# Kernel tuning notes

Hardware: AMD Instinct MI355X
Metric: run time of the kernel (lower is better)

The kernel has to match this reference:

```python
import jax, jax.numpy as jnp
import numpy as np

N_NODES = 100000
N_EDGES = 1600000
IN_FEATS = 128
HID = 128
OUT_FEATS = 64


def setup_inputs() -> dict:
    key = jax.random.key(0)
    ks = jax.random.split(key, 8)
    node_ids = jnp.arange(N_NODES, dtype=jnp.int64)
    src = jax.random.randint(ks[0], (N_EDGES,), 0, N_NODES, dtype=jnp.int64)
    dst = jax.random.randint(ks[1], (N_EDGES,), 0, N_NODES, dtype=jnp.int64)
    emb = jax.random.normal(ks[2], (N_NODES, IN_FEATS), dtype=jnp.float32)
    W1 = jax.random.normal(ks[3], (IN_FEATS, HID), dtype=jnp.float32) / np.sqrt(IN_FEATS)
    b1 = jnp.zeros((HID,), dtype=jnp.float32)
    W2 = jax.random.normal(ks[4], (HID, OUT_FEATS), dtype=jnp.float32) / np.sqrt(HID)
    b2 = jnp.zeros((OUT_FEATS,), dtype=jnp.float32)
    return {"node_ids": node_ids, "src": src, "dst": dst, "emb": emb,
            "W1": W1, "b1": b1, "W2": W2, "b2": b2}


def _sym_norms(src, dst):
    # DGL GraphConv norm='both': D_out^{-1/2} on source side, D_in^{-1/2} on dest side,
    # degrees clamped to >= 1.
    ones = jnp.ones(src.shape[0], dtype=jnp.float32)
    deg_out = jax.ops.segment_sum(ones, src, num_segments=N_NODES)
    deg_in = jax.ops.segment_sum(ones, dst, num_segments=N_NODES)
    norm_src = jnp.clip(deg_out, 1.0, None) ** -0.5  # [N]
    norm_dst = jnp.clip(deg_in, 1.0, None) ** -0.5   # [N]
    return norm_src, norm_dst


def _spmm(src, dst, h):
    # rst[dst] += h[src]  (sparse adjacency aggregation)
    return jax.ops.segment_sum(h[src], dst, num_segments=N_NODES)


def reference(node_ids, src, dst, emb, W1, b1, W2, b2):
    norm_src, norm_dst = _sym_norms(src, dst)
    h = emb[node_ids]                                   # [N, IN]
    # Layer 1 (IN -> HID, relu): weight applied after aggregation (in <= out)
    h = _spmm(src, dst, h * norm_src[:, None]) * norm_dst[:, None]
    h = jax.nn.relu(h @ W1 + b1)                        # [N, HID]
    # Dropout(0.5) is identity in eval mode.
    # Layer 2 (HID -> OUT): DGL applies weight BEFORE aggregation when in > out
    h = (h @ W2) * norm_src[:, None]                    # [N, OUT]
    h = _spmm(src, dst, h) * norm_dst[:, None] + b2
    return h
```

## Files before the change

### kernel.cpp

```cpp
#include <hip/hip_runtime.h>

#define N_N 100000
#define N_E 1600000
#define SLOTS 48
#define N_PAD 100096

#define BK_SHIFT 9
#define BK_SIZE 512
#define NBKT 196
#define MAXB 10240
#define EPB2 2048
#define NBLK2 ((N_E + EPB2 - 1) / EPB2)
#define EPT 8

#define EMBB 6250
#define WB 96

typedef unsigned short ushort_t;
typedef unsigned int uint_t;
typedef _Float16 f16x8 __attribute__((ext_vector_type(8)));
typedef float f32x4 __attribute__((ext_vector_type(4)));

__device__ __forceinline__ ushort_t f2h(float f) {
    union { _Float16 h; ushort_t u; } c; c.h = (_Float16)f; return c.u;
}

__device__ __forceinline__ void acc2h(uint_t v, float wv, float& a, float& b) {
    union { uint_t u; _Float16 h[2]; } c; c.u = v;
    a = fmaf((float)c.h[0], wv, a);
    b = fmaf((float)c.h[1], wv, b);
}

__device__ __forceinline__ void addh(uint_t v, float& a, float& b) {
    union { uint_t u; _Float16 h[2]; } c; c.u = v;
    a += (float)c.h[0];
    b += (float)c.h[1];
}

__device__ __forceinline__ uint_t packh2(float a, float b) {
    union { _Float16 h[2]; uint_t u; } p;
    p.h[0] = (_Float16)a; p.h[1] = (_Float16)b;
    return p.u;
}

__global__ void __launch_bounds__(256) k_scatter_prep(
        const int* __restrict__ src, const int* __restrict__ dst,
        int* __restrict__ cur_d, int* __restrict__ cur_s,
        uint_t* __restrict__ pe_dst, uint_t* __restrict__ pe_src,
        const float* __restrict__ emb, ushort_t* __restrict__ embf,
        const float* __restrict__ W1, const float* __restrict__ W2,
        ushort_t* __restrict__ w1f, ushort_t* __restrict__ w2f) {
    int t = threadIdx.x, blk = blockIdx.x;
    if (blk >= NBLK2) {
        int pb = blk - NBLK2;
        if (pb < EMBB) {
            int i = pb * 512 + t;
            const float4* E4 = (const float4*)emb;
            ushort4* O4 = (ushort4*)embf;
            float4 v0 = E4[i], v1 = E4[i + 256];
            ushort4 o0, o1;
            o0.x = f2h(v0.x); o0.y = f2h(v0.y); o0.z = f2h(v0.z); o0.w = f2h(v0.w);
            o1.x = f2h(v1.x); o1.y = f2h(v1.y); o1.z = f2h(v1.z); o1.w = f2h(v1.w);
            O4[i] = o0; O4[i + 256] = o1;
        } else {
            int idx = (pb - EMBB) * 256 + t;
            int j = idx & 7, l = (idx >> 3) & 63;
            int k = (l >> 4) * 8 + j;
            int n = l & 15;
            if (idx < 16384) {
                int kc = (idx >> 9) & 3, nt = idx >> 11;
                w1f[idx] = f2h(W1[(kc * 32 + k) * 128 + nt * 16 + n]);
            } else {
                int i2 = idx - 16384;
                int kc = (i2 >> 9) & 3, nt = i2 >> 11;
                w2f[i2] = f2h(W2[(kc * 32 + k) * 64 + nt * 16 + n]);
            }
        }
        return;
    }
    __shared__ int hd[NBKT], hs[NBKT], od[NBKT], os_[NBKT];
    for (int i = t; i < NBKT; i += 256) { hd[i] = 0; hs[i] = 0; }
    __syncthreads();
    int e0 = blk * EPB2;
    int myS[EPT], myD[EPT];
    uint_t myR[EPT];
#pragma unroll
    for (int i = 0; i < EPT; i++) {
        int e = e0 + t + i * 256;
        if (e < N_E) {
            int s = src[e], d = dst[e];
            myS[i] = s; myD[i] = d;
            uint_t rd = (uint_t)atomicAdd(&hd[d >> BK_SHIFT], 1);
            uint_t rs = (uint_t)atomicAdd(&hs[s >> BK_SHIFT], 1);
            myR[i] = rd | (rs << 16);
        }
    }
    __syncthreads();
    for (int i = t; i < NBKT; i += 256) {
        int c = hd[i]; od[i]  = c ? atomicAdd(&cur_d[i], c) : 0;
        c = hs[i];     os_[i] = c ? atomicAdd(&cur_s[i], c) : 0;
    }
    __syncthreads();
#pragma unroll
    for (int i = 0; i < EPT; i++) {
        int e = e0 + t + i * 256;
        if (e < N_E) {
            int s = myS[i], d = myD[i];
            int rd = od[d >> BK_SHIFT] + (int)(myR[i] & 0xffffu);
            int rs = os_[s >> BK_SHIFT] + (int)(myR[i] >> 16);
            if (rd < MAXB) pe_dst[(size_t)(d >> BK_SHIFT) * MAXB + rd] =
                               (uint_t)s | ((uint_t)(d & 511) << 17);
            if (rs < MAXB) pe_src[(size_t)(s >> BK_SHIFT) * MAXB + rs] = (uint_t)s;
        }
    }
}

__global__ void __launch_bounds__(512) k_binC(
        const uint_t* __restrict__ pe_dst, const uint_t* __restrict__ pe_src,
        const int* __restrict__ cur_d, const int* __restrict__ cur_s,
        int* __restrict__ slots, int* __restrict__ cnt,
        float* __restrict__ nd, float* __restrict__ ns) {
    int t = threadIdx.x, bb = blockIdx.x;
    __shared__ int lc[BK_SIZE];
    for (int i = t; i < BK_SIZE; i += 512) lc[i] = 0;
    __syncthreads();
    if (bb < NBKT) {
        int b = bb;
        int cb = min(cur_d[b], MAXB);
        int nbase = b << BK_SHIFT;
        const uint_t* pe = pe_dst + (size_t)b * MAXB;
        for (int e = t; e < cb; e += 512) {
            uint_t ed = pe[e];
            int dloc = (int)(ed >> 17);
            int s = (int)(ed & 0x1ffffu);
            int pos = atomicAdd(&lc[dloc], 1);
            if (pos < SLOTS) slots[(size_t)(nbase + dloc) * SLOTS + pos] = s;
        }
        __syncthreads();
        for (int i = t; i < BK_SIZE; i += 512) {
            int n = nbase + i;
            if (n < N_N) {
                int c = lc[i];
                cnt[n] = c;
                nd[n] = 1.0f / sqrtf((float)max(c, 1));
            }
        }
    } else {
        int b = bb - NBKT;
        int cb = min(cur_s[b], MAXB);
        int nbase = b << BK_SHIFT;
        const uint_t* pe = pe_src + (size_t)b * MAXB;
        for (int e = t; e < cb; e += 512)
            atomicAdd(&lc[(int)pe[e] - nbase], 1);
        __syncthreads();
        for (int i = t; i < BK_SIZE; i += 512) {
            int n = nbase + i;
            if (n < N_N) ns[n] = 1.0f / sqrtf((float)max(lc[i], 1));
        }
    }
}

__global__ void __launch_bounds__(256) k_spmm1(
        const int* __restrict__ cnt, const int* __restrict__ slots,
        const ushort_t* __restrict__ embf, const float* __restrict__ ns,
        const float* __restrict__ nd, uint_t* __restrict__ aggf) {
    int wid = (blockIdx.x * 256 + (int)threadIdx.x) >> 6;
    int node = __builtin_amdgcn_readfirstlane(wid);
    if (node >= N_N) return;
    int lane = threadIdx.x & 63;
    const int* row = slots + node * SLOTS;
    int len = min(cnt[node], SLOTS);
    float ax0 = 0.f, ay0 = 0.f, ax1 = 0.f, ay1 = 0.f;
    int e = 0;
    int n8 = len & ~7;
    for (; e < n8; e += 8) {
        int s0 = __builtin_amdgcn_readfirstlane(row[e + 0]);
        int s1 = __builtin_amdgcn_readfirstlane(row[e + 1]);
        int s2 = __builtin_amdgcn_readfirstlane(row[e + 2]);
        int s3 = __builtin_amdgcn_readfirstlane(row[e + 3]);
        int s4 = __builtin_amdgcn_readfirstlane(row[e + 4]);
        int s5 = __builtin_amdgcn_readfirstlane(row[e + 5]);
        int s6 = __builtin_amdgcn_readfirstlane(row[e + 6]);
        int s7 = __builtin_amdgcn_readfirstlane(row[e + 7]);
        float w0 = ns[s0], w1 = ns[s1], w2 = ns[s2], w3 = ns[s3];
        float w4 = ns[s4], w5 = ns[s5], w6 = ns[s6], w7 = ns[s7];
        uint_t v0 = ((const uint_t*)(embf + (size_t)s0 * 128))[lane];
        uint_t v1 = ((const uint_t*)(embf + (size_t)s1 * 128))[lane];
        uint_t v2 = ((const uint_t*)(embf + (size_t)s2 * 128))[lane];
        uint_t v3 = ((const uint_t*)(embf + (size_t)s3 * 128))[lane];
        uint_t v4 = ((const uint_t*)(embf + (size_t)s4 * 128))[lane];
        uint_t v5 = ((const uint_t*)(embf + (size_t)s5 * 128))[lane];
        uint_t v6 = ((const uint_t*)(embf + (size_t)s6 * 128))[lane];
        uint_t v7 = ((const uint_t*)(embf + (size_t)s7 * 128))[lane];
        acc2h(v0, w0, ax0, ay0);
        acc2h(v1, w1, ax1, ay1);
        acc2h(v2, w2, ax0, ay0);
        acc2h(v3, w3, ax1, ay1);
        acc2h(v4, w4, ax0, ay0);
        acc2h(v5, w5, ax1, ay1);
        acc2h(v6, w6, ax0, ay0);
        acc2h(v7, w7, ax1, ay1);
    }
    int n4 = len & ~3;
    for (; e < n4; e += 4) {
        int s0 = __builtin_amdgcn_readfirstlane(row[e + 0]);
        int s1 = __builtin_amdgcn_readfirstlane(row[e + 1]);
        int s2 = __builtin_amdgcn_readfirstlane(row[e + 2]);
        int s3 = __builtin_amdgcn_readfirstlane(row[e + 3]);
        float w0 = ns[s0], w1 = ns[s1], w2 = ns[s2], w3 = ns[s3];
        uint_t v0 = ((const uint_t*)(embf + (size_t)s0 * 128))[lane];
        uint_t v1 = ((const uint_t*)(embf + (size_t)s1 * 128))[lane];
        uint_t v2 = ((const uint_t*)(embf + (size_t)s2 * 128))[lane];
        uint_t v3 = ((const uint_t*)(embf + (size_t)s3 * 128))[lane];
        acc2h(v0, w0, ax0, ay0);
        acc2h(v1, w1, ax1, ay1);
        acc2h(v2, w2, ax0, ay0);
        acc2h(v3, w3, ax1, ay1);
    }
    for (; e < len; ++e) {
        int s = __builtin_amdgcn_readfirstlane(row[e]);
        float w = ns[s];
        uint_t v = ((const uint_t*)(embf + (size_t)s * 128))[lane];
        acc2h(v, w, ax0, ay0);
    }
    float sc = nd[node];
    aggf[(size_t)node * 64 + lane] = packh2((ax0 + ax1) * sc, (ay0 + ay1) * sc);
}

#define HSTH 136
__global__ void __launch_bounds__(256, 2) k_gemm(
        const ushort_t* __restrict__ aggf, const ushort_t* __restrict__ w1f,
        const float* __restrict__ b1, const ushort_t* __restrict__ w2f,
        const float* __restrict__ ns, ushort_t* __restrict__ h2b) {
    __shared__ ushort_t sh[128 * HSTH];
    int t = threadIdx.x;
    int w = t >> 6, l = t & 63;
    int quad = l >> 4, lm = l & 15;
    int nb0 = blockIdx.x * 128;

    f16x8 a[2][4];
#pragma unroll
    for (int rt = 0; rt < 2; rt++)
#pragma unroll
        for (int kc = 0; kc < 4; kc++)
            a[rt][kc] = *(const f16x8*)(aggf
                + (size_t)(nb0 + rt * 64 + w * 16 + lm) * 128 + kc * 32 + quad * 8);

    f32x4 acc[2][8];
#pragma unroll
    for (int rt = 0; rt < 2; rt++)
#pragma unroll
        for (int nt = 0; nt < 8; nt++) acc[rt][nt] = (f32x4){0.f, 0.f, 0.f, 0.f};

#pragma unroll
    for (int kc = 0; kc < 4; kc++) {
        f16x8 bq[8];
#pragma unroll
        for (int nt = 0; nt < 8; nt++)
            bq[nt] = *(const f16x8*)(w1f + (((nt * 4 + kc) * 64 + l) << 3));
#pragma unroll
        for (int nt = 0; nt < 8; nt++) {
            acc[0][nt] = __builtin_amdgcn_mfma_f32_16x16x32_f16(a[0][kc], bq[nt], acc[0][nt], 0, 0, 0);
            acc[1][nt] = __builtin_amdgcn_mfma_f32_16x16x32_f16(a[1][kc], bq[nt], acc[1][nt], 0, 0, 0);
        }
    }
#pragma unroll
    for (int nt = 0; nt < 8; nt++) {
        float bb = b1[nt * 16 + lm];
#pragma unroll
        for (int rt = 0; rt < 2; rt++)
#pragma unroll
            for (int r = 0; r < 4; r++) {
                int row = rt * 64 + w * 16 + quad * 4 + r;
                sh[row * HSTH + nt * 16 + lm] = f2h(fmaxf(acc[rt][nt][r] + bb, 0.f));
            }
    }
    __syncthreads();

    f16x8 hh[2][4];
#pragma unroll
    for (int rt = 0; rt < 2; rt++)
#pragma unroll
        for (int kc = 0; kc < 4; kc++)
            hh[rt][kc] = *(const f16x8*)(sh + (rt * 64 + w * 16 + lm) * HSTH
                                         + kc * 32 + quad * 8);

    f32x4 acc2[2][4];
#pragma unroll
    for (int rt = 0; rt < 2; rt++)
#pragma unroll
        for (int q = 0; q < 4; q++) acc2[rt][q] = (f32x4){0.f, 0.f, 0.f, 0.f};

#pragma unroll
    for (int kc = 0; kc < 4; kc++) {
        f16x8 b2q[4];
#pragma unroll
        for (int q = 0; q < 4; q++)
            b2q[q] = *(const f16x8*)(w2f + (((q * 4 + kc) * 64 + l) << 3));
#pragma unroll
        for (int q = 0; q < 4; q++) {
            acc2[0][q] = __builtin_amdgcn_mfma_f32_16x16x32_f16(hh[0][kc], b2q[q], acc2[0][q], 0, 0, 0);
            acc2[1][q] = __builtin_amdgcn_mfma_f32_16x16x32_f16(hh[1][kc], b2q[q], acc2[1][q], 0, 0, 0);
        }
    }
#pragma unroll
    for (int rt = 0; rt < 2; rt++)
#pragma unroll
        for (int r = 0; r < 4; r++) {
            int node = nb0 + rt * 64 + w * 16 + quad * 4 + r;
            if (node < N_N) {
                float s = ns[node];
#pragma unroll
                for (int q = 0; q < 4; q++)
                    h2b[(size_t)node * 64 + q * 16 + lm] = f2h(acc2[rt][q][r] * s);
            }
        }
}

__global__ void __launch_bounds__(256) k_spmm2(
        const int* __restrict__ cnt, const int* __restrict__ slots,
        const ushort_t* __restrict__ h2b, const float* __restrict__ nd,
        const float* __restrict__ b2, float* __restrict__ out) {
    int wid = (blockIdx.x * 256 + (int)threadIdx.x) >> 6;
    int node = __builtin_amdgcn_readfirstlane(wid);
    if (node >= N_N) return;
    int lane = threadIdx.x & 63;
    int q = lane >> 4, w16 = lane & 15;
    const int* row = slots + node * SLOTS;
    int len = min(cnt[node], SLOTS);
    const uint2* H2 = (const uint2*)h2b;
    float a0 = 0.f, a1 = 0.f, a2 = 0.f, a3 = 0.f;
    int e = 0;
    int n16 = len & ~15;
    for (; e < n16; e += 16) {
        const int* rp = row + e + q;
        int s0 = rp[0], s1 = rp[4], s2 = rp[8], s3 = rp[12];
        uint2 v0 = H2[(size_t)s0 * 16 + w16];
        uint2 v1 = H2[(size_t)s1 * 16 + w16];
        uint2 v2 = H2[(size_t)s2 * 16 + w16];
        uint2 v3 = H2[(size_t)s3 * 16 + w16];
        addh(v0.x, a0, a1); addh(v0.y, a2, a3);
        addh(v1.x, a0, a1); addh(v1.y, a2, a3);
        addh(v2.x, a0, a1); addh(v2.y, a2, a3);
        addh(v3.x, a0, a1); addh(v3.y, a2, a3);
    }
    int n4 = len & ~3;
    for (; e < n4; e += 4) {
        int s = row[e + q];
        uint2 v = H2[(size_t)s * 16 + w16];
        addh(v.x, a0, a1); addh(v.y, a2, a3);
    }
    if (e < len && q < len - e) {
        int s = row[e + q];
        uint2 v = H2[(size_t)s * 16 + w16];
        addh(v.x, a0, a1); addh(v.y, a2, a3);
    }
    a0 += __shfl_xor(a0, 16); a1 += __shfl_xor(a1, 16);
    a2 += __shfl_xor(a2, 16); a3 += __shfl_xor(a3, 16);
    a0 += __shfl_xor(a0, 32); a1 += __shfl_xor(a1, 32);
    a2 += __shfl_xor(a2, 32); a3 += __shfl_xor(a3, 32);
    if (q == 0) {
        float sc = nd[node];
        float4 bb = ((const float4*)b2)[w16];
        float4 o;
        o.x = a0 * sc + bb.x;
        o.y = a1 * sc + bb.y;
        o.z = a2 * sc + bb.z;
        o.w = a3 * sc + bb.w;
        ((float4*)(out + (size_t)node * 64))[w16] = o;
    }
}

extern "C" void kernel_launch(void* const* d_in, const int* in_sizes, int n_in,
                              void* d_out, int out_size, void* d_ws, size_t ws_size,
                              hipStream_t stream) {
    const int* src = (const int*)d_in[1];
    const int* dst = (const int*)d_in[2];
    const float* emb = (const float*)d_in[3];
    const float* W1 = (const float*)d_in[4];
    const float* b1 = (const float*)d_in[5];
    const float* W2 = (const float*)d_in[6];
    const float* b2 = (const float*)d_in[7];
    float* out = (float*)d_out;

    int* cur_d   = (int*)d_ws;
    int* cur_s   = cur_d + 256;
    int* cnt     = cur_s + 256;
    float* ns    = (float*)(cnt + N_PAD);
    float* nd    = ns + N_PAD;
    int* slots   = (int*)(nd + N_PAD);
    uint_t* pe_dst = (uint_t*)(slots + (size_t)N_N * SLOTS);
    uint_t* pe_src = pe_dst + (size_t)NBKT * MAXB;
    ushort_t* embf = (ushort_t*)(pe_src + (size_t)NBKT * MAXB);
    uint_t* aggf = (uint_t*)(embf + (size_t)N_PAD * 128);
    ushort_t* w1f = (ushort_t*)(aggf + (size_t)N_PAD * 64);
    ushort_t* w2f = w1f + 16384;
    ushort_t* h2b = w2f + 8192;

    hipMemsetAsync(cur_d, 0, sizeof(int) * 512, stream);
    k_scatter_prep<<<NBLK2 + EMBB + WB, 256, 0, stream>>>(
        src, dst, cur_d, cur_s, pe_dst, pe_src, emb, embf, W1, W2, w1f, w2f);
    k_binC  <<<2 * NBKT, 512, 0, stream>>>(
        pe_dst, pe_src, cur_d, cur_s, slots, cnt, nd, ns);
    k_spmm1 <<<(N_N + 3) / 4, 256, 0, stream>>>(cnt, slots, embf, ns, nd, aggf);
    k_gemm  <<<N_PAD / 128, 256, 0, stream>>>((const ushort_t*)aggf, w1f, b1, w2f, ns, h2b);
    k_spmm2 <<<(N_N + 3) / 4, 256, 0, stream>>>(cnt, slots, h2b, nd, b2, out);
}
```

Measured before the change: 298.3 us.

## Halve bucket size, stage slot table in LDS, cache weights in LDS for GEMM

Destination buckets shrink from 512 to 256 nodes, doubling the number of binning blocks. Each bucket's fixed-stride slot table is now built in shared memory and written to global memory with coalesced 16-byte stores, replacing scattered per-edge writes. The GEMM kernel handles 64 rows per block instead of 128 and first copies both weight matrices into shared memory, so it no longer reads them from global memory per wave. The tradeoffs are about 48KB of LDS per binning block, which limits occupancy, and copying the whole slot table even where slots are unused.

```diff
diff --git a/kernel.cpp b/kernel.cpp
--- a/kernel.cpp
+++ b/kernel.cpp
@@ -5,10 +5,10 @@
 #define SLOTS 48
 #define N_PAD 100096
 
-#define BK_SHIFT 9
-#define BK_SIZE 512
-#define NBKT 196
-#define MAXB 10240
+#define BK_SHIFT 8
+#define BK_SIZE 256
+#define NBKT 391
+#define MAXB 5120
 #define EPB2 2048
 #define NBLK2 ((N_E + EPB2 - 1) / EPB2)
 #define EPT 8
@@ -109,7 +109,7 @@
             int rd = od[d >> BK_SHIFT] + (int)(myR[i] & 0xffffu);
             int rs = os_[s >> BK_SHIFT] + (int)(myR[i] >> 16);
             if (rd < MAXB) pe_dst[(size_t)(d >> BK_SHIFT) * MAXB + rd] =
-                               (uint_t)s | ((uint_t)(d & 511) << 17);
+                               (uint_t)s | ((uint_t)(d & 255) << 17);
             if (rs < MAXB) pe_src[(size_t)(s >> BK_SHIFT) * MAXB + rs] = (uint_t)s;
         }
     }
@@ -122,6 +122,7 @@
         float* __restrict__ nd, float* __restrict__ ns) {
     int t = threadIdx.x, bb = blockIdx.x;
     __shared__ int lc[BK_SIZE];
+    __shared__ int sslot[BK_SIZE * SLOTS];
     for (int i = t; i < BK_SIZE; i += 512) lc[i] = 0;
     __syncthreads();
     if (bb < NBKT) {
@@ -134,9 +135,12 @@
             int dloc = (int)(ed >> 17);
             int s = (int)(ed & 0x1ffffu);
             int pos = atomicAdd(&lc[dloc], 1);
-            if (pos < SLOTS) slots[(size_t)(nbase + dloc) * SLOTS + pos] = s;
+            if (pos < SLOTS) sslot[dloc * SLOTS + pos] = s;
         }
         __syncthreads();
+        const uint4* S4 = (const uint4*)sslot;
+        uint4* G4 = (uint4*)(slots + (size_t)nbase * SLOTS);
+        for (int i = t; i < BK_SIZE * SLOTS / 4; i += 512) G4[i] = S4[i];
         for (int i = t; i < BK_SIZE; i += 512) {
             int n = nbase + i;
             if (n < N_N) {
@@ -168,7 +172,7 @@
     int node = __builtin_amdgcn_readfirstlane(wid);
     if (node >= N_N) return;
     int lane = threadIdx.x & 63;
-    const int* row = slots + node * SLOTS;
+    const int* row = slots + (size_t)node * SLOTS;
     int len = min(cnt[node], SLOTS);
     float ax0 = 0.f, ay0 = 0.f, ax1 = 0.f, ay1 = 0.f;
     int e = 0;
@@ -228,93 +232,84 @@
 }
 
 #define HSTH 136
-__global__ void __launch_bounds__(256, 2) k_gemm(
+__global__ void __launch_bounds__(256) k_gemm(
         const ushort_t* __restrict__ aggf, const ushort_t* __restrict__ w1f,
         const float* __restrict__ b1, const ushort_t* __restrict__ w2f,
         const float* __restrict__ ns, ushort_t* __restrict__ h2b) {
-    __shared__ ushort_t sh[128 * HSTH];
+    __shared__ ushort_t w1s[16384];
+    __shared__ ushort_t w2s[8192];
+    __shared__ ushort_t sh[64 * HSTH];
     int t = threadIdx.x;
     int w = t >> 6, l = t & 63;
     int quad = l >> 4, lm = l & 15;
-    int nb0 = blockIdx.x * 128;
-
-    f16x8 a[2][4];
-#pragma unroll
-    for (int rt = 0; rt < 2; rt++)
-#pragma unroll
-        for (int kc = 0; kc < 4; kc++)
-            a[rt][kc] = *(const f16x8*)(aggf
-                + (size_t)(nb0 + rt * 64 + w * 16 + lm) * 128 + kc * 32 + quad * 8);
-
-    f32x4 acc[2][8];
-#pragma unroll
-    for (int rt = 0; rt < 2; rt++)
-#pragma unroll
-        for (int nt = 0; nt < 8; nt++) acc[rt][nt] = (f32x4){0.f, 0.f, 0.f, 0.f};
-
+    int nb0 = blockIdx.x * 64;
+
+    {
+        uint4* d1 = (uint4*)w1s; const uint4* g1 = (const uint4*)w1f;
+        for (int i = t; i < 2048; i += 256) d1[i] = g1[i];
+        uint4* d2 = (uint4*)w2s; const uint4* g2 = (const uint4*)w2f;
+        for (int i = t; i < 1024; i += 256) d2[i] = g2[i];
+    }
+
+    f16x8 a[4];
+#pragma unroll
+    for (int kc = 0; kc < 4; kc++)
+        a[kc] = *(const f16x8*)(aggf
+            + (size_t)(nb0 + w * 16 + lm) * 128 + kc * 32 + quad * 8);
+    __syncthreads();
+
+    f32x4 acc[8];
+#pragma unroll
+    for (int nt = 0; nt < 8; nt++) acc[nt] = (f32x4){0.f, 0.f, 0.f, 0.f};
 #pragma unroll
     for (int kc = 0; kc < 4; kc++) {
         f16x8 bq[8];
 #pragma unroll
         for (int nt = 0; nt < 8; nt++)
-            bq[nt] = *(const f16x8*)(w1f + (((nt * 4 + kc) * 64 + l) << 3));
-#pragma unroll
-        for (int nt = 0; nt < 8; nt++) {
-            acc[0][nt] = __builtin_amdgcn_mfma_f32_16x16x32_f16(a[0][kc], bq[nt], acc[0][nt], 0, 0, 0);
-            acc[1][nt] = __builtin_amdgcn_mfma_f32_16x16x32_f16(a[1][kc], bq[nt], acc[1][nt], 0, 0, 0);
-        }
+            bq[nt] = *(const f16x8*)(w1s + (((nt * 4 + kc) * 64 + l) << 3));
+#pragma unroll
+        for (int nt = 0; nt < 8; nt++)
+            acc[nt] = __builtin_amdgcn_mfma_f32_16x16x32_f16(a[kc], bq[nt], acc[nt], 0, 0, 0);
     }
 #pragma unroll
     for (int nt = 0; nt < 8; nt++) {
         float bb = b1[nt * 16 + lm];
 #pragma unroll
-        for (int rt = 0; rt < 2; rt++)
-#pragma unroll
-            for (int r = 0; r < 4; r++) {
-                int row = rt * 64 + w * 16 + quad * 4 + r;
-                sh[row * HSTH + nt * 16 + lm] = f2h(fmaxf(acc[rt][nt][r] + bb, 0.f));
-            }
-    }
-    __syncthreads();
-
-    f16x8 hh[2][4];
-#pragma unroll
-    for (int rt = 0; rt < 2; rt++)
-#pragma unroll
-        for (int kc = 0; kc < 4; kc++)
-            hh[rt][kc] = *(const f16x8*)(sh + (rt * 64 + w * 16 + lm) * HSTH
-                                         + kc * 32 + quad * 8);
-
-    f32x4 acc2[2][4];
-#pragma unroll
-    for (int rt = 0; rt < 2; rt++)
-#pragma unroll
-        for (int q = 0; q < 4; q++) acc2[rt][q] = (f32x4){0.f, 0.f, 0.f, 0.f};
-
+        for (int r = 0; r < 4; r++) {
+            int row = w * 16 + quad * 4 + r;
+            sh[row * HSTH + nt * 16 + lm] = f2h(fmaxf(acc[nt][r] + bb, 0.f));
+        }
+    }
+    __syncthreads();
+
+    f16x8 hh[4];
+#pragma unroll
+    for (int kc = 0; kc < 4; kc++)
+        hh[kc] = *(const f16x8*)(sh + (w * 16 + lm) * HSTH + kc * 32 + quad * 8);
+
+    f32x4 acc2[4];
+#pragma unroll
+    for (int q = 0; q < 4; q++) acc2[q] = (f32x4){0.f, 0.f, 0.f, 0.f};
 #pragma unroll
     for (int kc = 0; kc < 4; kc++) {
         f16x8 b2q[4];
 #pragma unroll
         for (int q = 0; q < 4; q++)
-            b2q[q] = *(const f16x8*)(w2f + (((q * 4 + kc) * 64 + l) << 3));
-#pragma unroll
-        for (int q = 0; q < 4; q++) {
-            acc2[0][q] = __builtin_amdgcn_mfma_f32_16x16x32_f16(hh[0][kc], b2q[q], acc2[0][q], 0, 0, 0);
-            acc2[1][q] = __builtin_amdgcn_mfma_f32_16x16x32_f16(hh[1][kc], b2q[q], acc2[1][q], 0, 0, 0);
-        }
-    }
-#pragma unroll
-    for (int rt = 0; rt < 2; rt++)
-#pragma unroll
-        for (int r = 0; r < 4; r++) {
-            int node = nb0 + rt * 64 + w * 16 + quad * 4 + r;
-            if (node < N_N) {
-                float s = ns[node];
-#pragma unroll
-                for (int q = 0; q < 4; q++)
-                    h2b[(size_t)node * 64 + q * 16 + lm] = f2h(acc2[rt][q][r] * s);
-            }
-        }
+            b2q[q] = *(const f16x8*)(w2s + (((q * 4 + kc) * 64 + l) << 3));
+#pragma unroll
+        for (int q = 0; q < 4; q++)
+            acc2[q] = __builtin_amdgcn_mfma_f32_16x16x32_f16(hh[kc], b2q[q], acc2[q], 0, 0, 0);
+    }
+#pragma unroll
+    for (int r = 0; r < 4; r++) {
+        int node = nb0 + w * 16 + quad * 4 + r;
+        if (node < N_N) {
+            float s = ns[node];
+#pragma unroll
+            for (int q = 0; q < 4; q++)
+                h2b[(size_t)node * 64 + q * 16 + lm] = f2h(acc2[q][r] * s);
+        }
+    }
 }
 
 __global__ void __launch_bounds__(256) k_spmm2(
@@ -326,7 +321,7 @@
     if (node >= N_N) return;
     int lane = threadIdx.x & 63;
     int q = lane >> 4, w16 = lane & 15;
-    const int* row = slots + node * SLOTS;
+    const int* row = slots + (size_t)node * SLOTS;
     int len = min(cnt[node], SLOTS);
     const uint2* H2 = (const uint2*)h2b;
     float a0 = 0.f, a1 = 0.f, a2 = 0.f, a3 = 0.f;
@@ -384,12 +379,12 @@
     float* out = (float*)d_out;
 
     int* cur_d   = (int*)d_ws;
-    int* cur_s   = cur_d + 256;
-    int* cnt     = cur_s + 256;
+    int* cur_s   = cur_d + 512;
+    int* cnt     = cur_s + 512;
     float* ns    = (float*)(cnt + N_PAD);
     float* nd    = ns + N_PAD;
     int* slots   = (int*)(nd + N_PAD);
-    uint_t* pe_dst = (uint_t*)(slots + (size_t)N_N * SLOTS);
+    uint_t* pe_dst = (uint_t*)(slots + (size_t)N_PAD * SLOTS);
     uint_t* pe_src = pe_dst + (size_t)NBKT * MAXB;
     ushort_t* embf = (ushort_t*)(pe_src + (size_t)NBKT * MAXB);
     uint_t* aggf = (uint_t*)(embf + (size_t)N_PAD * 128);
@@ -397,12 +392,12 @@
     ushort_t* w2f = w1f + 16384;
     ushort_t* h2b = w2f + 8192;
 
-    hipMemsetAsync(cur_d, 0, sizeof(int) * 512, stream);
+    hipMemsetAsync(cur_d, 0, sizeof(int) * 1024, stream);
     k_scatter_prep<<<NBLK2 + EMBB + WB, 256, 0, stream>>>(
         src, dst, cur_d, cur_s, pe_dst, pe_src, emb, embf, W1, W2, w1f, w2f);
     k_binC  <<<2 * NBKT, 512, 0, stream>>>(
         pe_dst, pe_src, cur_d, cur_s, slots, cnt, nd, ns);
     k_spmm1 <<<(N_N + 3) / 4, 256, 0, stream>>>(cnt, slots, embf, ns, nd, aggf);
-    k_gemm  <<<N_PAD / 128, 256, 0, stream>>>((const ushort_t*)aggf, w1f, b1, w2f, ns, h2b);
+    k_gemm  <<<N_PAD / 64, 256, 0, stream>>>((const ushort_t*)aggf, w1f, b1, w2f, ns, h2b);
     k_spmm2 <<<(N_N + 3) / 4, 256, 0, stream>>>(cnt, slots, h2b, nd, b2, out);
 }
```

After: 285.7 us. -4.2%, faster.
